# Performance work log

Hardware: AMD Instinct MI355X
Metric: run time of the kernel (lower is better)

Reference implementation:

```python
import jax, jax.numpy as jnp
import numpy as np

B, T, C, H = 128, 256, 512, 2048
STEP_SIZE = 0.001
TOTAL = 1.0 / (T - 1)                       # uniform linspace(0,1,T) interval length
STEPS_HINT = max(1, int(TOTAL / STEP_SIZE))
N_SUB = max(1, int(max(STEPS_HINT, TOTAL / STEP_SIZE)))  # = 3 fixed RK4 substeps per interval
DT = TOTAL / N_SUB


def setup_inputs() -> dict:
    key = jax.random.key(0)
    ks = jax.random.split(key, 7)
    def lin_w(k, fi, fo):
        return (jax.random.uniform(k, (fi, fo), jnp.float32, -1.0, 1.0) / np.sqrt(fi)).astype(jnp.float32)
    def lin_b(k, fi, fo):
        return (jax.random.uniform(k, (fo,), jnp.float32, -1.0, 1.0) / np.sqrt(fi)).astype(jnp.float32)
    x = jax.random.normal(ks[0], (B, T, C), jnp.float32)
    return {
        "x": x,
        "W1": lin_w(ks[1], C, H), "b1": lin_b(ks[2], C, H),
        "W2": lin_w(ks[3], H, H), "b2": lin_b(ks[4], H, H),
        "W3": lin_w(ks[5], H, C), "b3": lin_b(ks[6], H, C),
    }


def _mlp(y, W1, b1, W2, b2, W3, b3):
    # f(y) = Linear(Tanh(Linear(Tanh(Linear(y)))))
    h = jnp.tanh(y @ W1 + b1)
    h = jnp.tanh(h @ W2 + b2)
    return h @ W3 + b3


def _rk4_step(y, dt, p):
    k1 = _mlp(y, *p)
    k2 = _mlp(y + 0.5 * dt * k1, *p)
    k3 = _mlp(y + 0.5 * dt * k2, *p)
    k4 = _mlp(y + dt * k3, *p)
    return y + (dt / 6.0) * (k1 + 2.0 * k2 + 2.0 * k3 + k4)


def reference(x, W1, b1, W2, b2, W3, b3):
    p = (W1, b1, W2, b2, W3, b3)
    def interval(y, _):
        for _ in range(N_SUB):  # static, small unroll (3)
            y = _rk4_step(y, DT, p)
        return y, y
    y0 = x[:, 0, :]                                   # [B, C]
    _, ys = jax.lax.scan(interval, y0, None, length=T - 1)  # ys: [T-1, B, C]
    return jnp.concatenate([x[:, :1, :], jnp.moveaxis(ys, 0, 1)], axis=1)  # [B, T, C]
```

## Files before the change

kernel.cpp:

```cpp
#include <hip/hip_runtime.h>
#include <hip/hip_bf16.h>
#include <cstdint>

#define B_ 128
#define T_ 256
#define C_ 512
#define H_ 2048
#define NWG 256
#define NTHR 256
#define NGROUP 8
#define GSIZE 32
#define M_ 16
#define FSTRIDE 16
#define RSU1 132
#define RSS1 528
#define DT_F 0.0013071895424836601f
#define POLL_CAP 8192

typedef __bf16 bf16x8 __attribute__((ext_vector_type(8)));
typedef short s16x8 __attribute__((ext_vector_type(8)));
typedef float f32x4 __attribute__((ext_vector_type(4)));
typedef unsigned long long ull;

enum : size_t {
  OFF_FLAGS = 0,
  OFF_SHAD  = 16384,
  OFF_PROBE = 32768,
  OFF_OK    = 49152,
  OFF_W1P   = 65536,
  OFF_W2P = OFF_W1P + (size_t)C_ * H_ * 2,
  OFF_W3P = OFF_W2P + (size_t)H_ * H_ * 2,
  OFF_U   = OFF_W3P + (size_t)H_ * C_ * 2,
  OFF_H1  = OFF_U   + (size_t)NGROUP * M_ * C_ * 2,
  OFF_H2  = OFF_H1  + (size_t)NGROUP * M_ * H_ * 2,
  WS_END  = OFF_H2  + (size_t)NGROUP * M_ * H_ * 2
};

__device__ __forceinline__ bf16x8 ld_frag(const unsigned short* p) {
  s16x8 v = *reinterpret_cast<const s16x8*>(p);
  return __builtin_bit_cast(bf16x8, v);
}
__device__ __forceinline__ bf16x8 lds_frag(const unsigned short* p) {
  s16x8 v = *reinterpret_cast<const s16x8*>(p);
  return __builtin_bit_cast(bf16x8, v);
}
__device__ __forceinline__ void st16(unsigned short* p, unsigned short v, bool fast) {
  if (fast) *p = v;
  else __hip_atomic_store(p, v, __ATOMIC_RELAXED, __HIP_MEMORY_SCOPE_AGENT);
}
__device__ __forceinline__ f32x4 mfma16(bf16x8 a, bf16x8 b, f32x4 c) {
  return __builtin_amdgcn_mfma_f32_16x16x32_bf16(a, b, c, 0, 0, 0);
}
__device__ __forceinline__ unsigned short tobf(float f) {
  return __builtin_bit_cast(unsigned short, (__bf16)f);
}
__device__ __forceinline__ float fast_tanh(float v) {
  float e = __expf(2.0f * v);
  return 1.0f - 2.0f / (e + 1.0f);
}
__device__ __forceinline__ unsigned ld_sc0_u32(const unsigned* p) {
  unsigned v;
  asm volatile("global_load_dword %0, %1, off sc0\n\t"
               "s_waitcnt vmcnt(0)"
               : "=&v"(v) : "v"(p) : "memory");
  return v;
}
__device__ __forceinline__ void issue8f(const ull* base, unsigned o0, unsigned stride, ull v[8]) {
  unsigned a0 = o0,            a1 = o0 + stride,     a2 = o0 + 2 * stride, a3 = o0 + 3 * stride,
           a4 = o0 + 4 * stride, a5 = o0 + 5 * stride, a6 = o0 + 6 * stride, a7 = o0 + 7 * stride;
  asm volatile(
      "global_load_dwordx2 %0, %8, %16 sc0\n\t"
      "global_load_dwordx2 %1, %9, %16 sc0\n\t"
      "global_load_dwordx2 %2, %10, %16 sc0\n\t"
      "global_load_dwordx2 %3, %11, %16 sc0\n\t"
      "global_load_dwordx2 %4, %12, %16 sc0\n\t"
      "global_load_dwordx2 %5, %13, %16 sc0\n\t"
      "global_load_dwordx2 %6, %14, %16 sc0\n\t"
      "global_load_dwordx2 %7, %15, %16 sc0\n\t"
      "s_waitcnt vmcnt(0)"
      : "=&v"(v[0]), "=&v"(v[1]), "=&v"(v[2]), "=&v"(v[3]),
        "=&v"(v[4]), "=&v"(v[5]), "=&v"(v[6]), "=&v"(v[7])
      : "v"(a0), "v"(a1), "v"(a2), "v"(a3), "v"(a4), "v"(a5), "v"(a6), "v"(a7),
        "s"(base)
      : "memory");
}

__global__ void init_flags_k(unsigned* f) {
  int i = blockIdx.x * 256 + threadIdx.x;
  if (i < 16384) f[i] = 0u;
}

__global__ void swizzle_w_k(const float* __restrict__ W, unsigned short* __restrict__ Wp,
                            int N, int kblog) {
  int idx = blockIdx.x * 256 + threadIdx.x;
  int j = idx & 7;
  int l = (idx >> 3) & 63;
  int rem = idx >> 9;
  int kb = rem & ((1 << kblog) - 1);
  int nt = rem >> kblog;
  int k = kb * 32 + ((l >> 4) << 3) + j;
  int n = (nt << 4) + (l & 15);
  Wp[idx] = tobf(W[(size_t)k * N + n]);
}

__device__ __forceinline__ void bar_arrive(unsigned* gf, unsigned* gs, int gn,
                                           unsigned gen, bool fast) {
  asm volatile("s_waitcnt vmcnt(0)" ::: "memory");
  __syncthreads();
  if (threadIdx.x == 0) {
    if (fast) {
      gf[gn * FSTRIDE] = gen;
      __hip_atomic_store(&gs[gn * FSTRIDE], gen, __ATOMIC_RELAXED,
                         __HIP_MEMORY_SCOPE_AGENT);
    } else {
      __hip_atomic_store(&gf[gn * FSTRIDE], gen, __ATOMIC_RELAXED,
                         __HIP_MEMORY_SCOPE_AGENT);
    }
  }
}
__device__ __forceinline__ void bar_wait(unsigned* gf, unsigned* gs, unsigned gen,
                                         bool fast, bool& sticky) {
  if (threadIdx.x < GSIZE) {
    const unsigned* fp = gf + threadIdx.x * FSTRIDE;
    const unsigned* sp = gs + threadIdx.x * FSTRIDE;
    if (fast && !sticky) {
      int it = 0; bool done = false;
      for (;;) {
        if (ld_sc0_u32(fp) >= gen) { done = true; break; }
        if (++it > POLL_CAP) break;
        __builtin_amdgcn_s_sleep(1);
      }
      if (!done) {
        while (__hip_atomic_load(sp, __ATOMIC_RELAXED, __HIP_MEMORY_SCOPE_AGENT) < gen)
          __builtin_amdgcn_s_sleep(2);
        if (ld_sc0_u32(fp) < gen) sticky = true;
      }
    } else if (fast) {
      while (__hip_atomic_load(sp, __ATOMIC_RELAXED, __HIP_MEMORY_SCOPE_AGENT) < gen)
        __builtin_amdgcn_s_sleep(1);
    } else {
      while (__hip_atomic_load(fp, __ATOMIC_RELAXED, __HIP_MEMORY_SCOPE_AGENT) < gen)
        __builtin_amdgcn_s_sleep(1);
    }
  }
  __syncthreads();
}

__device__ __forceinline__ void issue_u(const ull* __restrict__ g, int tid, ull v[8], bool fast) {
  if (fast) {
    issue8f(g, (unsigned)(tid * 8), 2048u, v);
  } else {
    #pragma unroll
    for (int j = 0; j < 8; ++j)
      v[j] = __hip_atomic_load(g + j * NTHR + tid, __ATOMIC_RELAXED, __HIP_MEMORY_SCOPE_AGENT);
  }
}
__device__ __forceinline__ void issue_c(const ull* __restrict__ g, int tid, ull v[8], bool fast) {
  if (fast) {
    unsigned o0 = (unsigned)((((tid >> 7) * 512) + (tid & 127)) * 8);
    issue8f(g, o0, 8192u, v);
  } else {
    #pragma unroll
    for (int j = 0; j < 8; ++j) {
      int i = j * NTHR + tid;
      v[j] = __hip_atomic_load(g + (size_t)(i >> 7) * 512 + (i & 127),
                               __ATOMIC_RELAXED, __HIP_MEMORY_SCOPE_AGENT);
    }
  }
}
__device__ __forceinline__ void commit(ull* __restrict__ lds, int tid, const ull v[8]) {
  #pragma unroll
  for (int j = 0; j < 8; ++j) {
    int i = j * NTHR + tid;
    lds[(i >> 7) * RSU1 + (i & 127)] = v[j];
  }
}

#define L2CHUNK(c, buf) {                                                     \
  const unsigned short* al = (const unsigned short*)atile[buf] + llo * RSS1 + lhi * 8; \
  _Pragma("unroll")                                                           \
  for (int jj = 0; jj < 8; ++jj) {                                            \
    acc0 = mfma16(lds_frag(al + (2 * jj) * 32),     w2r[(c) * 16 + 2 * jj],     acc0); \
    acc1 = mfma16(lds_frag(al + (2 * jj + 1) * 32), w2r[(c) * 16 + 2 * jj + 1], acc1); \
  } }

#define L3CHUNK(c, buf) {                                                     \
  const unsigned short* al = (const unsigned short*)atile[buf] + llo * RSS1 + lhi * 8; \
  _Pragma("unroll")                                                           \
  for (int jj = 0; jj < 2; ++jj) {                                            \
    acc0 = mfma16(lds_frag(al + (wave * 4 + 2 * jj) * 32),     w3r[(c) * 4 + 2 * jj],     acc0); \
    acc1 = mfma16(lds_frag(al + (wave * 4 + 2 * jj + 1) * 32), w3r[(c) * 4 + 2 * jj + 1], acc1); \
  } }

__global__ __launch_bounds__(NTHR, 1) void ode_persist_k(
    const float* __restrict__ x, const float* __restrict__ b1,
    const float* __restrict__ b2, const float* __restrict__ b3,
    float* __restrict__ out, unsigned char* __restrict__ ws) {
  const int wg = blockIdx.x, tid = threadIdx.x;
  const int g = wg & 7, gn = wg >> 3;
  const int wave = tid >> 6, lane = tid & 63;
  const int lhi = lane >> 4, llo = lane & 15;

  unsigned* gflags = (unsigned*)(ws + OFF_FLAGS) + g * GSIZE * FSTRIDE;
  unsigned* gshad  = (unsigned*)(ws + OFF_SHAD)  + g * GSIZE * FSTRIDE;
  unsigned* probe  = (unsigned*)(ws + OFF_PROBE) + g * GSIZE * FSTRIDE;
  unsigned* okarr  = (unsigned*)(ws + OFF_OK)    + g * GSIZE * FSTRIDE;
  const unsigned short* W1p = (const unsigned short*)(ws + OFF_W1P);
  const unsigned short* W2p = (const unsigned short*)(ws + OFF_W2P);
  const unsigned short* W3p = (const unsigned short*)(ws + OFF_W3P);
  const ull* ubuf_u = (const ull*)(ws + OFF_U)  + (size_t)g * (M_ * C_ / 4);
  const ull* h1_u   = (const ull*)(ws + OFF_H1) + (size_t)g * (M_ * H_ / 4);
  const ull* h2_u   = (const ull*)(ws + OFF_H2) + (size_t)g * (M_ * H_ / 4);
  unsigned short* ubuf_s = (unsigned short*)(ws + OFF_U)  + (size_t)g * M_ * C_;
  unsigned short* h1_s   = (unsigned short*)(ws + OFF_H1) + (size_t)g * M_ * H_;
  unsigned short* h2_s   = (unsigned short*)(ws + OFF_H2) + (size_t)g * M_ * H_;

  __shared__ alignas(16) ull atile[2][M_ * RSU1];
  __shared__ float red[4][256];
  __shared__ float ytile[256], k1t[256], k2t[256], k3t[256];
  __shared__ int sh_ok;

  const int n16 = gn * 4 + wave;
  const unsigned short* bp1 = W1p + (size_t)n16 * 16 * 512 + lane * 8;
  const unsigned short* bp2 = W2p + (size_t)n16 * 64 * 512 + lane * 8;
  const unsigned short* bp3 = W3p + (size_t)gn  * 64 * 512 + lane * 8;

  bf16x8 w2r[64], w3r[16];
  #pragma unroll
  for (int kb = 0; kb < 64; ++kb) w2r[kb] = ld_frag(bp2 + kb * 512);
  #pragma unroll
  for (int q = 0; q < 16; ++q)
    w3r[q] = ld_frag(bp3 + ((q >> 2) * 16 + wave * 4 + (q & 3)) * 512);

  const float bb1 = b1[n16 * 16 + llo];
  const float bb2 = b2[n16 * 16 + llo];
  const float bb3 = b3[gn * 16 + llo];

  {
    int row = tid >> 4, c16 = tid & 15;
    int col = gn * 16 + c16;
    int b = g * M_ + row;
    float v = x[(size_t)b * (T_ * C_) + col];
    ytile[tid] = v;
    out[(size_t)b * (T_ * C_) + col] = v;
    __hip_atomic_store(&ubuf_s[row * C_ + col], tobf(v),
                       __ATOMIC_RELAXED, __HIP_MEMORY_SCOPE_AGENT);
  }
  if (tid == 0) sh_ok = 1;
  if (tid == 1) probe[gn * FSTRIDE] = 0xA5A50000u | (unsigned)(g << 8) | (unsigned)gn;
  unsigned gen = 0;
  bool sticky = false;
  bar_arrive(gflags, gshad, gn, ++gen, false);
  bar_wait(gflags, gshad, gen, false, sticky);

  {
    bool myok = true;
    if (tid < GSIZE) {
      unsigned v = ld_sc0_u32(&probe[tid * FSTRIDE]);
      myok = (v == (0xA5A50000u | (unsigned)(g << 8) | (unsigned)tid));
    }
    __syncthreads();
    if (!myok) sh_ok = 0;
    __syncthreads();
    if (tid == 0)
      __hip_atomic_store(&okarr[gn * FSTRIDE], sh_ok ? 2u : 1u,
                         __ATOMIC_RELAXED, __HIP_MEMORY_SCOPE_AGENT);
  }
  bar_arrive(gflags, gshad, gn, ++gen, false);
  bar_wait(gflags, gshad, gen, false, sticky);
  {
    bool myok = true;
    if (tid < GSIZE)
      myok = (__hip_atomic_load(&okarr[tid * FSTRIDE], __ATOMIC_RELAXED,
                                __HIP_MEMORY_SCOPE_AGENT) == 2u);
    __syncthreads();
    if (!myok) sh_ok = 0;
    __syncthreads();
  }
  const bool fast = sh_ok != 0;

  ull va[8], vb[8];
  #pragma unroll 1
  for (int t = 0; t < T_ - 1; ++t) {
    #pragma unroll 1
    for (int sub = 0; sub < 3; ++sub) {
      #pragma unroll 1
      for (int st = 0; st < 4; ++st) {
        {
          issue_u(ubuf_u, tid, va, fast);
          bf16x8 w1f[16];
          #pragma unroll
          for (int kb = 0; kb < 16; ++kb) w1f[kb] = ld_frag(bp1 + kb * 512);
          commit(atile[0], tid, va);
          __syncthreads();
          f32x4 acc0 = {0.f, 0.f, 0.f, 0.f}, acc1 = {0.f, 0.f, 0.f, 0.f};
          const unsigned short* al = (const unsigned short*)atile[0] + llo * RSS1 + lhi * 8;
          #pragma unroll
          for (int jj = 0; jj < 8; ++jj) {
            acc0 = mfma16(lds_frag(al + (2 * jj) * 32),     w1f[2 * jj],     acc0);
            acc1 = mfma16(lds_frag(al + (2 * jj + 1) * 32), w1f[2 * jj + 1], acc1);
          }
          f32x4 a = acc0 + acc1;
          const int col = n16 * 16 + llo;
          #pragma unroll
          for (int r = 0; r < 4; ++r)
            st16(&h1_s[(lhi * 4 + r) * H_ + col], tobf(fast_tanh(a[r] + bb1)), fast);
        }
        bar_arrive(gflags, gshad, gn, ++gen, fast);
        bar_wait(gflags, gshad, gen, fast, sticky);

        {
          f32x4 acc0 = {0.f, 0.f, 0.f, 0.f}, acc1 = {0.f, 0.f, 0.f, 0.f};
          issue_c(h1_u,       tid, va, fast);
          issue_c(h1_u + 128, tid, vb, fast);
          commit(atile[0], tid, va);
          __syncthreads();
          issue_c(h1_u + 256, tid, va, fast);
          L2CHUNK(0, 0);
          commit(atile[1], tid, vb);
          __syncthreads();
          issue_c(h1_u + 384, tid, vb, fast);
          L2CHUNK(1, 1);
          commit(atile[0], tid, va);
          __syncthreads();
          L2CHUNK(2, 0);
          commit(atile[1], tid, vb);
          __syncthreads();
          L2CHUNK(3, 1);
          f32x4 a = acc0 + acc1;
          const int col = n16 * 16 + llo;
          #pragma unroll
          for (int r = 0; r < 4; ++r)
            st16(&h2_s[(lhi * 4 + r) * H_ + col], tobf(fast_tanh(a[r] + bb2)), fast);
        }
        bar_arrive(gflags, gshad, gn, ++gen, fast);
        bar_wait(gflags, gshad, gen, fast, sticky);

        {
          f32x4 acc0 = {0.f, 0.f, 0.f, 0.f}, acc1 = {0.f, 0.f, 0.f, 0.f};
          issue_c(h2_u,       tid, va, fast);
          issue_c(h2_u + 128, tid, vb, fast);
          commit(atile[0], tid, va);
          __syncthreads();
          issue_c(h2_u + 256, tid, va, fast);
          L3CHUNK(0, 0);
          commit(atile[1], tid, vb);
          __syncthreads();
          issue_c(h2_u + 384, tid, vb, fast);
          L3CHUNK(1, 1);
          commit(atile[0], tid, va);
          __syncthreads();
          L3CHUNK(2, 0);
          commit(atile[1], tid, vb);
          __syncthreads();
          L3CHUNK(3, 1);
          f32x4 a = acc0 + acc1;
          #pragma unroll
          for (int r = 0; r < 4; ++r) red[wave][(lhi * 4 + r) * 16 + llo] = a[r];
          __syncthreads();
          if (wave == 0) {
            const float dt = DT_F;
            #pragma unroll
            for (int r = 0; r < 4; ++r) {
              int row = lhi * 4 + r;
              int i = row * 16 + llo;
              float z = red[0][i] + red[1][i] + red[2][i] + red[3][i] + bb3;
              float yv = ytile[i];
              unsigned short* up = &ubuf_s[row * C_ + gn * 16 + llo];
              if (st == 0)      { k1t[i] = z; st16(up, tobf(yv + 0.5f * dt * z), fast); }
              else if (st == 1) { k2t[i] = z; st16(up, tobf(yv + 0.5f * dt * z), fast); }
              else if (st == 2) { k3t[i] = z; st16(up, tobf(yv + dt * z), fast); }
              else {
                float yn = yv + (dt * (1.0f / 6.0f)) * (k1t[i] + 2.f * k2t[i] + 2.f * k3t[i] + z);
                ytile[i] = yn;
                st16(up, tobf(yn), fast);
                if (sub == 2)
                  out[(size_t)(g * M_ + row) * (T_ * C_) + (size_t)(t + 1) * C_ + gn * 16 + llo] = yn;
              }
            }
          }
        }
        bar_arrive(gflags, gshad, gn, ++gen, fast);
        bar_wait(gflags, gshad, gen, fast, sticky);
      }
    }
  }
}

extern "C" void kernel_launch(void* const* d_in, const int* in_sizes, int n_in,
                              void* d_out, int out_size, void* d_ws, size_t ws_size,
                              hipStream_t stream) {
  (void)in_sizes; (void)n_in; (void)out_size; (void)ws_size;
  const float* x  = (const float*)d_in[0];
  const float* W1 = (const float*)d_in[1];
  const float* b1 = (const float*)d_in[2];
  const float* W2 = (const float*)d_in[3];
  const float* b2 = (const float*)d_in[4];
  const float* W3 = (const float*)d_in[5];
  const float* b3 = (const float*)d_in[6];
  float* out = (float*)d_out;
  unsigned char* ws = (unsigned char*)d_ws;

  init_flags_k<<<64, 256, 0, stream>>>((unsigned*)(ws + OFF_FLAGS));
  swizzle_w_k<<<(C_ * H_) / 256, 256, 0, stream>>>(W1, (unsigned short*)(ws + OFF_W1P), H_, 4);
  swizzle_w_k<<<(H_ * H_) / 256, 256, 0, stream>>>(W2, (unsigned short*)(ws + OFF_W2P), H_, 6);
  swizzle_w_k<<<(H_ * C_) / 256, 256, 0, stream>>>(W3, (unsigned short*)(ws + OFF_W3P), C_, 6);

  ode_persist_k<<<NWG, NTHR, 0, stream>>>(x, b1, b2, b3, out, ws);
}
```

Baseline: 49.62 ms.

## Pack barrier flags densely, spin without sleep, and overlap async loads with MFMA

The fast-path group barrier now writes its flags into a packed per-group array instead of cacheline-strided slots, and the pollers spin without s_sleep so they react sooner. The global loads of activation chunks no longer wait inside the asm block. Explicit vmcnt waits let the next chunk's loads stay in flight while MFMAs run on the current LDS tile, and the full __syncthreads is replaced by an lgkmcnt wait plus s_barrier. The risks are more memory traffic from busy polling, and false sharing since 32 flags now share cache lines.

```diff
diff --git a/kernel.cpp b/kernel.cpp
--- a/kernel.cpp
+++ b/kernel.cpp
@@ -27,7 +27,8 @@
   OFF_SHAD  = 16384,
   OFF_PROBE = 32768,
   OFF_OK    = 49152,
-  OFF_W1P   = 65536,
+  OFF_PF    = 65536,
+  OFF_W1P   = 69632,
   OFF_W2P = OFF_W1P + (size_t)C_ * H_ * 2,
   OFF_W3P = OFF_W2P + (size_t)H_ * H_ * 2,
   OFF_U   = OFF_W3P + (size_t)H_ * C_ * 2,
@@ -65,9 +66,17 @@
                : "=&v"(v) : "v"(p) : "memory");
   return v;
 }
-__device__ __forceinline__ void issue8f(const ull* base, unsigned o0, unsigned stride, ull v[8]) {
-  unsigned a0 = o0,            a1 = o0 + stride,     a2 = o0 + 2 * stride, a3 = o0 + 3 * stride,
-           a4 = o0 + 4 * stride, a5 = o0 + 5 * stride, a6 = o0 + 6 * stride, a7 = o0 + 7 * stride;
+#define WAITVM(N) asm volatile("s_waitcnt vmcnt(" #N ")" ::: "memory")
+#define LGKM0_BAR() do {                                   \
+  asm volatile("s_waitcnt lgkmcnt(0)" ::: "memory");       \
+  __builtin_amdgcn_s_barrier();                            \
+} while (0)
+
+__device__ __forceinline__ void issue8f_nw(const ull* base, unsigned o0, unsigned stride,
+                                           ull v[8]) {
+  unsigned a0 = o0,              a1 = o0 + stride,     a2 = o0 + 2 * stride,
+           a3 = o0 + 3 * stride, a4 = o0 + 4 * stride, a5 = o0 + 5 * stride,
+           a6 = o0 + 6 * stride, a7 = o0 + 7 * stride;
   asm volatile(
       "global_load_dwordx2 %0, %8, %16 sc0\n\t"
       "global_load_dwordx2 %1, %9, %16 sc0\n\t"
@@ -76,8 +85,7 @@
       "global_load_dwordx2 %4, %12, %16 sc0\n\t"
       "global_load_dwordx2 %5, %13, %16 sc0\n\t"
       "global_load_dwordx2 %6, %14, %16 sc0\n\t"
-      "global_load_dwordx2 %7, %15, %16 sc0\n\t"
-      "s_waitcnt vmcnt(0)"
+      "global_load_dwordx2 %7, %15, %16 sc0"
       : "=&v"(v[0]), "=&v"(v[1]), "=&v"(v[2]), "=&v"(v[3]),
         "=&v"(v[4]), "=&v"(v[5]), "=&v"(v[6]), "=&v"(v[7])
       : "v"(a0), "v"(a1), "v"(a2), "v"(a3), "v"(a4), "v"(a5), "v"(a6), "v"(a7),
@@ -87,7 +95,7 @@
 
 __global__ void init_flags_k(unsigned* f) {
   int i = blockIdx.x * 256 + threadIdx.x;
-  if (i < 16384) f[i] = 0u;
+  if (i < 17408) f[i] = 0u;
 }
 
 __global__ void swizzle_w_k(const float* __restrict__ W, unsigned short* __restrict__ Wp,
@@ -103,13 +111,13 @@
   Wp[idx] = tobf(W[(size_t)k * N + n]);
 }
 
-__device__ __forceinline__ void bar_arrive(unsigned* gf, unsigned* gs, int gn,
-                                           unsigned gen, bool fast) {
+__device__ __forceinline__ void bar_arrive(unsigned* gf, unsigned* gs, unsigned* pf,
+                                           int gn, unsigned gen, bool fast) {
   asm volatile("s_waitcnt vmcnt(0)" ::: "memory");
   __syncthreads();
   if (threadIdx.x == 0) {
     if (fast) {
-      gf[gn * FSTRIDE] = gen;
+      pf[gn] = gen;
       __hip_atomic_store(&gs[gn * FSTRIDE], gen, __ATOMIC_RELAXED,
                          __HIP_MEMORY_SCOPE_AGENT);
     } else {
@@ -118,17 +126,16 @@
     }
   }
 }
-__device__ __forceinline__ void bar_wait(unsigned* gf, unsigned* gs, unsigned gen,
-                                         bool fast, bool& sticky) {
+__device__ __forceinline__ void bar_wait(unsigned* gf, unsigned* gs, unsigned* pf,
+                                         unsigned gen, bool fast, bool& sticky) {
   if (threadIdx.x < GSIZE) {
-    const unsigned* fp = gf + threadIdx.x * FSTRIDE;
     const unsigned* sp = gs + threadIdx.x * FSTRIDE;
     if (fast && !sticky) {
+      const unsigned* fp = pf + threadIdx.x;
       int it = 0; bool done = false;
       for (;;) {
         if (ld_sc0_u32(fp) >= gen) { done = true; break; }
         if (++it > POLL_CAP) break;
-        __builtin_amdgcn_s_sleep(1);
       }
       if (!done) {
         while (__hip_atomic_load(sp, __ATOMIC_RELAXED, __HIP_MEMORY_SCOPE_AGENT) < gen)
@@ -139,6 +146,7 @@
       while (__hip_atomic_load(sp, __ATOMIC_RELAXED, __HIP_MEMORY_SCOPE_AGENT) < gen)
         __builtin_amdgcn_s_sleep(1);
     } else {
+      const unsigned* fp = gf + threadIdx.x * FSTRIDE;
       while (__hip_atomic_load(fp, __ATOMIC_RELAXED, __HIP_MEMORY_SCOPE_AGENT) < gen)
         __builtin_amdgcn_s_sleep(1);
     }
@@ -146,26 +154,17 @@
   __syncthreads();
 }
 
-__device__ __forceinline__ void issue_u(const ull* __restrict__ g, int tid, ull v[8], bool fast) {
-  if (fast) {
-    issue8f(g, (unsigned)(tid * 8), 2048u, v);
-  } else {
-    #pragma unroll
-    for (int j = 0; j < 8; ++j)
-      v[j] = __hip_atomic_load(g + j * NTHR + tid, __ATOMIC_RELAXED, __HIP_MEMORY_SCOPE_AGENT);
-  }
-}
-__device__ __forceinline__ void issue_c(const ull* __restrict__ g, int tid, ull v[8], bool fast) {
-  if (fast) {
-    unsigned o0 = (unsigned)((((tid >> 7) * 512) + (tid & 127)) * 8);
-    issue8f(g, o0, 8192u, v);
-  } else {
-    #pragma unroll
-    for (int j = 0; j < 8; ++j) {
-      int i = j * NTHR + tid;
-      v[j] = __hip_atomic_load(g + (size_t)(i >> 7) * 512 + (i & 127),
-                               __ATOMIC_RELAXED, __HIP_MEMORY_SCOPE_AGENT);
-    }
+__device__ __forceinline__ void issue_u_slow(const ull* __restrict__ g, int tid, ull v[8]) {
+  #pragma unroll
+  for (int j = 0; j < 8; ++j)
+    v[j] = __hip_atomic_load(g + j * NTHR + tid, __ATOMIC_RELAXED, __HIP_MEMORY_SCOPE_AGENT);
+}
+__device__ __forceinline__ void issue_c_slow(const ull* __restrict__ g, int tid, ull v[8]) {
+  #pragma unroll
+  for (int j = 0; j < 8; ++j) {
+    int i = j * NTHR + tid;
+    v[j] = __hip_atomic_load(g + (size_t)(i >> 7) * 512 + (i & 127),
+                             __ATOMIC_RELAXED, __HIP_MEMORY_SCOPE_AGENT);
   }
 }
 __device__ __forceinline__ void commit(ull* __restrict__ lds, int tid, const ull v[8]) {
@@ -205,6 +204,7 @@
   unsigned* gshad  = (unsigned*)(ws + OFF_SHAD)  + g * GSIZE * FSTRIDE;
   unsigned* probe  = (unsigned*)(ws + OFF_PROBE) + g * GSIZE * FSTRIDE;
   unsigned* okarr  = (unsigned*)(ws + OFF_OK)    + g * GSIZE * FSTRIDE;
+  unsigned* pflag  = (unsigned*)(ws + OFF_PF)    + g * 64;
   const unsigned short* W1p = (const unsigned short*)(ws + OFF_W1P);
   const unsigned short* W2p = (const unsigned short*)(ws + OFF_W2P);
   const unsigned short* W3p = (const unsigned short*)(ws + OFF_W3P);
@@ -250,8 +250,8 @@
   if (tid == 1) probe[gn * FSTRIDE] = 0xA5A50000u | (unsigned)(g << 8) | (unsigned)gn;
   unsigned gen = 0;
   bool sticky = false;
-  bar_arrive(gflags, gshad, gn, ++gen, false);
-  bar_wait(gflags, gshad, gen, false, sticky);
+  bar_arrive(gflags, gshad, pflag, gn, ++gen, false);
+  bar_wait(gflags, gshad, pflag, gen, false, sticky);
 
   {
     bool myok = true;
@@ -266,8 +266,8 @@
       __hip_atomic_store(&okarr[gn * FSTRIDE], sh_ok ? 2u : 1u,
                          __ATOMIC_RELAXED, __HIP_MEMORY_SCOPE_AGENT);
   }
-  bar_arrive(gflags, gshad, gn, ++gen, false);
-  bar_wait(gflags, gshad, gen, false, sticky);
+  bar_arrive(gflags, gshad, pflag, gn, ++gen, false);
+  bar_wait(gflags, gshad, pflag, gen, false, sticky);
   {
     bool myok = true;
     if (tid < GSIZE)
@@ -279,6 +279,7 @@
   }
   const bool fast = sh_ok != 0;
 
+  const unsigned o0c = (unsigned)((((tid >> 7) * 512) + (tid & 127)) * 8);
   ull va[8], vb[8];
   #pragma unroll 1
   for (int t = 0; t < T_ - 1; ++t) {
@@ -287,13 +288,22 @@
       #pragma unroll 1
       for (int st = 0; st < 4; ++st) {
         {
-          issue_u(ubuf_u, tid, va, fast);
+          f32x4 acc0 = {0.f, 0.f, 0.f, 0.f}, acc1 = {0.f, 0.f, 0.f, 0.f};
           bf16x8 w1f[16];
-          #pragma unroll
-          for (int kb = 0; kb < 16; ++kb) w1f[kb] = ld_frag(bp1 + kb * 512);
-          commit(atile[0], tid, va);
-          __syncthreads();
-          f32x4 acc0 = {0.f, 0.f, 0.f, 0.f}, acc1 = {0.f, 0.f, 0.f, 0.f};
+          if (fast) {
+            issue8f_nw(ubuf_u, (unsigned)(tid * 8), 2048u, va);
+            #pragma unroll
+            for (int kb = 0; kb < 16; ++kb) w1f[kb] = ld_frag(bp1 + kb * 512);
+            WAITVM(0);
+            commit(atile[0], tid, va);
+            LGKM0_BAR();
+          } else {
+            issue_u_slow(ubuf_u, tid, va);
+            #pragma unroll
+            for (int kb = 0; kb < 16; ++kb) w1f[kb] = ld_frag(bp1 + kb * 512);
+            commit(atile[0], tid, va);
+            __syncthreads();
+          }
           const unsigned short* al = (const unsigned short*)atile[0] + llo * RSS1 + lhi * 8;
           #pragma unroll
           for (int jj = 0; jj < 8; ++jj) {
@@ -306,54 +316,100 @@
           for (int r = 0; r < 4; ++r)
             st16(&h1_s[(lhi * 4 + r) * H_ + col], tobf(fast_tanh(a[r] + bb1)), fast);
         }
-        bar_arrive(gflags, gshad, gn, ++gen, fast);
-        bar_wait(gflags, gshad, gen, fast, sticky);
+        bar_arrive(gflags, gshad, pflag, gn, ++gen, fast);
+        bar_wait(gflags, gshad, pflag, gen, fast, sticky);
 
         {
           f32x4 acc0 = {0.f, 0.f, 0.f, 0.f}, acc1 = {0.f, 0.f, 0.f, 0.f};
-          issue_c(h1_u,       tid, va, fast);
-          issue_c(h1_u + 128, tid, vb, fast);
-          commit(atile[0], tid, va);
-          __syncthreads();
-          issue_c(h1_u + 256, tid, va, fast);
-          L2CHUNK(0, 0);
-          commit(atile[1], tid, vb);
-          __syncthreads();
-          issue_c(h1_u + 384, tid, vb, fast);
-          L2CHUNK(1, 1);
-          commit(atile[0], tid, va);
-          __syncthreads();
-          L2CHUNK(2, 0);
-          commit(atile[1], tid, vb);
-          __syncthreads();
-          L2CHUNK(3, 1);
+          if (fast) {
+            issue8f_nw(h1_u,       o0c, 8192u, va);
+            issue8f_nw(h1_u + 128, o0c, 8192u, vb);
+            WAITVM(8);
+            commit(atile[0], tid, va);
+            LGKM0_BAR();
+            issue8f_nw(h1_u + 256, o0c, 8192u, va);
+            L2CHUNK(0, 0);
+            WAITVM(8);
+            commit(atile[1], tid, vb);
+            LGKM0_BAR();
+            issue8f_nw(h1_u + 384, o0c, 8192u, vb);
+            L2CHUNK(1, 1);
+            WAITVM(8);
+            commit(atile[0], tid, va);
+            LGKM0_BAR();
+            L2CHUNK(2, 0);
+            WAITVM(0);
+            commit(atile[1], tid, vb);
+            LGKM0_BAR();
+            L2CHUNK(3, 1);
+          } else {
+            issue_c_slow(h1_u,       tid, va);
+            issue_c_slow(h1_u + 128, tid, vb);
+            commit(atile[0], tid, va);
+            __syncthreads();
+            issue_c_slow(h1_u + 256, tid, va);
+            L2CHUNK(0, 0);
+            commit(atile[1], tid, vb);
+            __syncthreads();
+            issue_c_slow(h1_u + 384, tid, vb);
+            L2CHUNK(1, 1);
+            commit(atile[0], tid, va);
+            __syncthreads();
+            L2CHUNK(2, 0);
+            commit(atile[1], tid, vb);
+            __syncthreads();
+            L2CHUNK(3, 1);
+          }
           f32x4 a = acc0 + acc1;
           const int col = n16 * 16 + llo;
           #pragma unroll
           for (int r = 0; r < 4; ++r)
             st16(&h2_s[(lhi * 4 + r) * H_ + col], tobf(fast_tanh(a[r] + bb2)), fast);
         }
-        bar_arrive(gflags, gshad, gn, ++gen, fast);
-        bar_wait(gflags, gshad, gen, fast, sticky);
+        bar_arrive(gflags, gshad, pflag, gn, ++gen, fast);
+        bar_wait(gflags, gshad, pflag, gen, fast, sticky);
 
         {
           f32x4 acc0 = {0.f, 0.f, 0.f, 0.f}, acc1 = {0.f, 0.f, 0.f, 0.f};
-          issue_c(h2_u,       tid, va, fast);
-          issue_c(h2_u + 128, tid, vb, fast);
-          commit(atile[0], tid, va);
-          __syncthreads();
-          issue_c(h2_u + 256, tid, va, fast);
-          L3CHUNK(0, 0);
-          commit(atile[1], tid, vb);
-          __syncthreads();
-          issue_c(h2_u + 384, tid, vb, fast);
-          L3CHUNK(1, 1);
-          commit(atile[0], tid, va);
-          __syncthreads();
-          L3CHUNK(2, 0);
-          commit(atile[1], tid, vb);
-          __syncthreads();
-          L3CHUNK(3, 1);
+          if (fast) {
+            issue8f_nw(h2_u,       o0c, 8192u, va);
+            issue8f_nw(h2_u + 128, o0c, 8192u, vb);
+            WAITVM(8);
+            commit(atile[0], tid, va);
+            LGKM0_BAR();
+            issue8f_nw(h2_u + 256, o0c, 8192u, va);
+            L3CHUNK(0, 0);
+            WAITVM(8);
+            commit(atile[1], tid, vb);
+            LGKM0_BAR();
+            issue8f_nw(h2_u + 384, o0c, 8192u, vb);
+            L3CHUNK(1, 1);
+            WAITVM(8);
+            commit(atile[0], tid, va);
+            LGKM0_BAR();
+            L3CHUNK(2, 0);
+            WAITVM(0);
+            commit(atile[1], tid, vb);
+            LGKM0_BAR();
+            L3CHUNK(3, 1);
+          } else {
+            issue_c_slow(h2_u,       tid, va);
+            issue_c_slow(h2_u + 128, tid, vb);
+            commit(atile[0], tid, va);
+            __syncthreads();
+            issue_c_slow(h2_u + 256, tid, va);
+            L3CHUNK(0, 0);
+            commit(atile[1], tid, vb);
+            __syncthreads();
+            issue_c_slow(h2_u + 384, tid, vb);
+            L3CHUNK(1, 1);
+            commit(atile[0], tid, va);
+            __syncthreads();
+            L3CHUNK(2, 0);
+            commit(atile[1], tid, vb);
+            __syncthreads();
+            L3CHUNK(3, 1);
+          }
           f32x4 a = acc0 + acc1;
           #pragma unroll
           for (int r = 0; r < 4; ++r) red[wave][(lhi * 4 + r) * 16 + llo] = a[r];
@@ -380,8 +436,8 @@
             }
           }
         }
-        bar_arrive(gflags, gshad, gn, ++gen, fast);
-        bar_wait(gflags, gshad, gen, fast, sticky);
+        bar_arrive(gflags, gshad, pflag, gn, ++gen, fast);
+        bar_wait(gflags, gshad, pflag, gen, fast, sticky);
       }
     }
   }
@@ -401,7 +457,7 @@
   float* out = (float*)d_out;
   unsigned char* ws = (unsigned char*)d_ws;
 
-  init_flags_k<<<64, 256, 0, stream>>>((unsigned*)(ws + OFF_FLAGS));
+  init_flags_k<<<68, 256, 0, stream>>>((unsigned*)(ws + OFF_FLAGS));
   swizzle_w_k<<<(C_ * H_) / 256, 256, 0, stream>>>(W1, (unsigned short*)(ws + OFF_W1P), H_, 4);
   swizzle_w_k<<<(H_ * H_) / 256, 256, 0, stream>>>(W2, (unsigned short*)(ws + OFF_W2P), H_, 6);
   swizzle_w_k<<<(H_ * C_) / 256, 256, 0, stream>>>(W3, (unsigned short*)(ws + OFF_W3P), C_, 6);
```

Measured after the change: 56.31 ms. 1.13x slower.
